# Kernel optimization log

Measured on AMD Instinct MI355X. Metric: run time of the kernel, lower is better.

The kernel has to match this reference:

```python
import jax, jax.numpy as jnp
import numpy as np

DIM = 512
HEADS = 8
HEAD_DIM = DIM // HEADS
SCALE = HEAD_DIM ** -0.5
GROUP1 = np.array([2, 3, 5, 6, 1, 4, 0, 7, 8, 9, 14, 15, 11, 12, 10, 13])
GROUP2 = np.array([0, 1, 2, 3, 5, 6, 4, 7])
EPS = 1e-5


def setup_inputs() -> dict:
    key = jax.random.key(0)
    ks = jax.random.split(key, 6)
    B, N, C = 4096, 16, DIM
    x = jax.random.normal(ks[0], (B, N, C), dtype=jnp.float32)
    w_q = jax.random.normal(ks[1], (C, C), dtype=jnp.float32) * 0.02
    w_kv = jax.random.normal(ks[2], (2 * C, C), dtype=jnp.float32) * 0.02
    w_proj = jax.random.normal(ks[3], (C, C), dtype=jnp.float32) * 0.02
    b_proj = jax.random.normal(ks[4], (C,), dtype=jnp.float32) * 0.02
    gamma = jnp.ones((C,), dtype=jnp.float32)
    beta = jnp.zeros((C,), dtype=jnp.float32)
    return {"x": x, "w_q": w_q, "w_kv": w_kv, "w_proj": w_proj,
            "b_proj": b_proj, "gamma": gamma, "beta": beta}


def _layernorm(x, gamma, beta):
    mu = jnp.mean(x, axis=-1, keepdims=True)
    var = jnp.mean(jnp.square(x - mu), axis=-1, keepdims=True)
    return (x - mu) * jax.lax.rsqrt(var + EPS) * gamma + beta


def _avg_pool_pairs(x):
    # x: (B, L, C) -> (B, L//2, C), AvgPool1d(kernel=2, stride=2) over L
    return 0.5 * (x[:, 0::2] + x[:, 1::2])


def reference(x, w_q, w_kv, w_proj, b_proj, gamma, beta):
    B, N, C = x.shape
    q = (x @ w_q.T).reshape(B, N, HEADS, HEAD_DIM).transpose(0, 2, 1, 3)  # (B,H,N,d)
    # gather + avgpool preprocessing
    p1 = _avg_pool_pairs(x[:, GROUP1])  # (B, 8, C)
    p2 = _avg_pool_pairs(x[:, GROUP2])  # (B, 4, C)
    pools = jnp.concatenate([x, p1, p2], axis=1)  # (B, N+12, C)
    pools = _layernorm(pools, gamma, beta)
    M = pools.shape[1]
    kv = (pools @ w_kv.T).reshape(B, M, 2, HEADS, HEAD_DIM).transpose(2, 0, 3, 1, 4)
    k, v = kv[0], kv[1]  # (B,H,M,d)
    attn = jax.nn.softmax(jnp.einsum('bhnd,bhmd->bhnm', q, k) * SCALE, axis=-1)
    out = jnp.einsum('bhnm,bhmd->bhnd', attn, v)  # (B,H,N,d)
    out = out.transpose(0, 2, 1, 3).reshape(B, N, C)
    return out @ w_proj.T + b_proj
```

## Files before the change

kernel.cpp:

```cpp
#include <hip/hip_runtime.h>
#include <hip/hip_bf16.h>
#include <cstdint>
#include <cstddef>


using bf16 = __hip_bfloat16;

#define B_SZ   4096
#define NTOK   16
#define CDIM   512
#define MPOOL  28
#define NHEAD  8
#define HDIM   64
#define LN_EPS 1e-5f
#define ATT_SCALE 0.125f

typedef short bf16x8 __attribute__((ext_vector_type(8)));
typedef float f32x4  __attribute__((ext_vector_type(4)));
typedef float f32x16 __attribute__((ext_vector_type(16)));

__constant__ int c_g1[16] = {2,3,5,6,1,4,0,7,8,9,14,15,11,12,10,13};
__constant__ int c_g2[8]  = {0,1,2,3,5,6,4,7};

__device__ __forceinline__ unsigned short f2b(float f) {
    unsigned u = __float_as_uint(f);
    return (unsigned short)((u + 0x7FFFu + ((u >> 16) & 1u)) >> 16);
}

__device__ __forceinline__ void lds_cp16(const void* g, void* l) {
    __builtin_amdgcn_global_load_lds(
        (const __attribute__((address_space(1))) void*)g,
        (__attribute__((address_space(3))) void*)l, 16, 0, 0);
}

__global__ __launch_bounds__(256) void convert_all_kernel(
    const float* __restrict__ w_q, const float* __restrict__ w_kv,
    const float* __restrict__ w_proj, bf16* __restrict__ wqb,
    bf16* __restrict__ wkvb, bf16* __restrict__ wpb)
{
    const float* src; bf16* dst; int i;
    const int blk = blockIdx.x;
    if (blk < 128)      { src = w_q;    dst = wqb; i = blk * 256 + threadIdx.x; }
    else if (blk < 384) { src = w_kv;   dst = wkvb; i = (blk - 128) * 256 + threadIdx.x; }
    else                { src = w_proj; dst = wpb; i = (blk - 384) * 256 + threadIdx.x; }
    const float4* p = (const float4*)(src + (size_t)i * 8);
    float4 a = p[0], b = p[1];
    uint4 pk;
    pk.x = (unsigned)f2b(a.x) | ((unsigned)f2b(a.y) << 16);
    pk.y = (unsigned)f2b(a.z) | ((unsigned)f2b(a.w) << 16);
    pk.z = (unsigned)f2b(b.x) | ((unsigned)f2b(b.y) << 16);
    pk.w = (unsigned)f2b(b.z) | ((unsigned)f2b(b.w) << 16);
    *(uint4*)(dst + (size_t)i * 8) = pk;
}

__global__ __launch_bounds__(256) void pools_ln_kernel(
    const float* __restrict__ x, const float* __restrict__ gamma,
    const float* __restrict__ beta, bf16* __restrict__ pools,
    bf16* __restrict__ xb)
{
    const int wave = threadIdx.x >> 6;
    const int lane = threadIdx.x & 63;
    const int row  = blockIdx.x * 4 + wave;
    const int b = row / MPOOL;
    const int m = row % MPOOL;
    const float* xb_src = x + (size_t)b * NTOK * CDIM;
    const int c0 = lane * 8;

    float v[8];
    if (m < 16) {
        const float4* p = (const float4*)(xb_src + m * CDIM + c0);
        float4 a = p[0], c = p[1];
        v[0]=a.x; v[1]=a.y; v[2]=a.z; v[3]=a.w;
        v[4]=c.x; v[5]=c.y; v[6]=c.z; v[7]=c.w;
        uint4 pk;
        pk.x = (unsigned)f2b(v[0]) | ((unsigned)f2b(v[1]) << 16);
        pk.y = (unsigned)f2b(v[2]) | ((unsigned)f2b(v[3]) << 16);
        pk.z = (unsigned)f2b(v[4]) | ((unsigned)f2b(v[5]) << 16);
        pk.w = (unsigned)f2b(v[6]) | ((unsigned)f2b(v[7]) << 16);
        *(uint4*)(xb + (size_t)b * NTOK * CDIM + (size_t)m * CDIM + c0) = pk;
    } else {
        int r0, r1;
        if (m < 24) { int j = m - 16; r0 = c_g1[2*j]; r1 = c_g1[2*j+1]; }
        else        { int j = m - 24; r0 = c_g2[2*j]; r1 = c_g2[2*j+1]; }
        const float4* p0 = (const float4*)(xb_src + r0 * CDIM + c0);
        const float4* p1 = (const float4*)(xb_src + r1 * CDIM + c0);
        float4 a0 = p0[0], a1 = p0[1];
        float4 b0 = p1[0], b1 = p1[1];
        v[0]=0.5f*(a0.x+b0.x); v[1]=0.5f*(a0.y+b0.y);
        v[2]=0.5f*(a0.z+b0.z); v[3]=0.5f*(a0.w+b0.w);
        v[4]=0.5f*(a1.x+b1.x); v[5]=0.5f*(a1.y+b1.y);
        v[6]=0.5f*(a1.z+b1.z); v[7]=0.5f*(a1.w+b1.w);
    }

    float s = 0.f, sq = 0.f;
#pragma unroll
    for (int j = 0; j < 8; ++j) { s += v[j]; sq += v[j]*v[j]; }
#pragma unroll
    for (int off = 1; off < 64; off <<= 1) {
        s  += __shfl_xor(s,  off, 64);
        sq += __shfl_xor(sq, off, 64);
    }
    const float mu   = s * (1.f / CDIM);
    const float var  = sq * (1.f / CDIM) - mu * mu;
    const float rstd = rsqrtf(var + LN_EPS);

    unsigned short o[8];
#pragma unroll
    for (int j = 0; j < 8; ++j) {
        float g  = gamma[c0 + j];
        float bb = beta[c0 + j];
        o[j] = f2b((v[j] - mu) * rstd * g + bb);
    }
    uint4 pk;
    pk.x = (unsigned)o[0] | ((unsigned)o[1] << 16);
    pk.y = (unsigned)o[2] | ((unsigned)o[3] << 16);
    pk.z = (unsigned)o[4] | ((unsigned)o[5] << 16);
    pk.w = (unsigned)o[6] | ((unsigned)o[7] << 16);
    *(uint4*)(pools + (size_t)row * CDIM + c0) = pk;
}

template<bool OUT_BF16, bool BIAS, int NBLK, bool FRAG32>
__global__ __launch_bounds__(512, 2) void gemm256_kernel(
    const bf16* __restrict__ A, const bf16* __restrict__ W,
    const float* __restrict__ bias, void* __restrict__ Cptr, int Ncols)
{
    constexpr int K  = 512;
    constexpr int NT = K / 32;
    extern __shared__ __align__(16) char ring[];

    const int tid = threadIdx.x;
    const int wv = tid >> 6, ln = tid & 63;
    const int wr = wv >> 2, wc = wv & 3;

    const int p  = blockIdx.x;
    const int o  = p >> 3;
    const int mb = (o / NBLK) * 8 + (p & 7);
    const int nb = o % NBLK;
    const size_t m0 = (size_t)mb * 256;
    const size_t n0 = (size_t)nb * 256;

    const int srow = wv * 16 + (ln >> 2);
    const int scol = (((ln & 3) * 16) ^ (((ln >> 3) & 3) << 4)) >> 1;
    const bf16* Asrc0 = A + (m0 + srow) * K + scol;
    const bf16* Asrc1 = A + (m0 + 128 + srow) * K + scol;
    const bf16* Wsrc0 = W + (n0 + srow) * K + scol;
    const bf16* Wsrc1 = W + (n0 + 128 + srow) * K + scol;
    char* const ringc = ring;

    auto STAGE = [&](int t) {
        char* base = ringc + (t & 3) * 32768 + wv * 1024;
        const int ko = t * 32;
        lds_cp16(Asrc0 + ko, base);
        lds_cp16(Asrc1 + ko, base + 8192);
        lds_cp16(Wsrc0 + ko, base + 16384);
        lds_cp16(Wsrc1 + ko, base + 16384 + 8192);
    };

    if constexpr (!FRAG32) {
        const int fr = ln & 15, kb = ln >> 4;
        const int aswz  = ((fr >> 1) & 3) << 4;
        const int a_off = (wr * 128 + fr) * 64 + ((kb * 16) ^ aswz);
        const int b_off = 16384 + (wc * 64 + fr) * 64 + ((kb * 16) ^ aswz);

        f32x4 acc[8][4];
#pragma unroll
        for (int i = 0; i < 8; ++i)
#pragma unroll
        for (int j = 0; j < 4; ++j)
            acc[i][j] = f32x4{0.f, 0.f, 0.f, 0.f};

        STAGE(0);
        STAGE(1);
        asm volatile("s_waitcnt vmcnt(4)" ::: "memory");
        __builtin_amdgcn_s_barrier();

#pragma unroll 1
        for (int t = 0; t < NT; ++t) {
            if (t + 2 < NT) STAGE(t + 2);
            const char* sa = ringc + (t & 3) * 32768;

            bf16x8 af[8], bfr[4];
#pragma unroll
            for (int mi = 0; mi < 8; ++mi)
                af[mi] = *(const bf16x8*)(sa + a_off + mi * 1024);
#pragma unroll
            for (int nj = 0; nj < 4; ++nj)
                bfr[nj] = *(const bf16x8*)(sa + b_off + nj * 1024);

#pragma unroll
            for (int mi = 0; mi < 8; ++mi)
#pragma unroll
            for (int nj = 0; nj < 4; ++nj)
                acc[mi][nj] = __builtin_amdgcn_mfma_f32_16x16x32_bf16(
                    af[mi], bfr[nj], acc[mi][nj], 0, 0, 0);

            if (t + 2 < NT) { asm volatile("s_waitcnt vmcnt(4)" ::: "memory"); }
            else            { asm volatile("s_waitcnt vmcnt(0)" ::: "memory"); }
            __builtin_amdgcn_s_barrier();
        }

        const int orow0 = wr * 128 + kb * 4;
        const int ocol0 = wc * 64 + fr;
        float bv[4];
#pragma unroll
        for (int nj = 0; nj < 4; ++nj)
            bv[nj] = BIAS ? bias[n0 + ocol0 + nj * 16] : 0.f;
#pragma unroll
        for (int mi = 0; mi < 8; ++mi) {
            const size_t rbase = m0 + orow0 + mi * 16;
#pragma unroll
            for (int r = 0; r < 4; ++r) {
                const size_t rowoff = (rbase + r) * (size_t)Ncols + n0 + ocol0;
#pragma unroll
                for (int nj = 0; nj < 4; ++nj) {
                    float v = acc[mi][nj][r] + bv[nj];
                    if (OUT_BF16)
                        ((unsigned short*)Cptr)[rowoff + nj * 16] = f2b(v);
                    else
                        ((float*)Cptr)[rowoff + nj * 16] = v;
                }
            }
        }
    } else {
        const int lnrow = ln & 31;
        const int khalf = ln >> 5;
        const int swz   = (((ln & 15) >> 1) & 3) << 4;
        const int a_base = (wr * 128 + lnrow) * 64;
        const int b_base = 16384 + (wc * 64 + lnrow) * 64;

        f32x16 acc[4][2];
#pragma unroll
        for (int i = 0; i < 4; ++i)
#pragma unroll
        for (int j = 0; j < 2; ++j)
#pragma unroll
            for (int e = 0; e < 16; ++e)
                acc[i][j][e] = 0.f;

        STAGE(0);
        STAGE(1);
        asm volatile("s_waitcnt vmcnt(4)" ::: "memory");
        __builtin_amdgcn_s_barrier();

#pragma unroll 1
        for (int t = 0; t < NT; ++t) {
            if (t + 2 < NT) STAGE(t + 2);
            const char* sa = ringc + (t & 3) * 32768;

            bf16x8 af[4][2], bfr[2][2];
#pragma unroll
            for (int mi = 0; mi < 4; ++mi)
#pragma unroll
                for (int ks = 0; ks < 2; ++ks)
                    af[mi][ks] = *(const bf16x8*)(sa + a_base + mi * 2048 +
                                     ((ks * 32 + khalf * 16) ^ swz));
#pragma unroll
            for (int nj = 0; nj < 2; ++nj)
#pragma unroll
                for (int ks = 0; ks < 2; ++ks)
                    bfr[nj][ks] = *(const bf16x8*)(sa + b_base + nj * 2048 +
                                     ((ks * 32 + khalf * 16) ^ swz));

#pragma unroll
            for (int mi = 0; mi < 4; ++mi)
#pragma unroll
            for (int nj = 0; nj < 2; ++nj) {
                acc[mi][nj] = __builtin_amdgcn_mfma_f32_32x32x16_bf16(
                    af[mi][0], bfr[nj][0], acc[mi][nj], 0, 0, 0);
                acc[mi][nj] = __builtin_amdgcn_mfma_f32_32x32x16_bf16(
                    af[mi][1], bfr[nj][1], acc[mi][nj], 0, 0, 0);
            }

            if (t + 2 < NT) { asm volatile("s_waitcnt vmcnt(4)" ::: "memory"); }
            else            { asm volatile("s_waitcnt vmcnt(0)" ::: "memory"); }
            __builtin_amdgcn_s_barrier();
        }

        const int ocol0 = wc * 64 + lnrow;
        float bv[2];
#pragma unroll
        for (int nj = 0; nj < 2; ++nj)
            bv[nj] = BIAS ? bias[n0 + ocol0 + nj * 32] : 0.f;
#pragma unroll
        for (int mi = 0; mi < 4; ++mi) {
            const size_t rbase = m0 + wr * 128 + mi * 32 + 4 * khalf;
#pragma unroll
            for (int r4 = 0; r4 < 4; ++r4) {
#pragma unroll
                for (int rl = 0; rl < 4; ++rl) {
                    const size_t rowoff = (rbase + rl + 8 * r4) * (size_t)Ncols
                                          + n0 + ocol0;
#pragma unroll
                    for (int nj = 0; nj < 2; ++nj) {
                        float v = acc[mi][nj][r4 * 4 + rl] + bv[nj];
                        if (OUT_BF16)
                            ((unsigned short*)Cptr)[rowoff + nj * 32] = f2b(v);
                        else
                            ((float*)Cptr)[rowoff + nj * 32] = v;
                    }
                }
            }
        }
    }
}

__global__ __launch_bounds__(256, 4) void attn_kernel(
    const bf16* __restrict__ q, const bf16* __restrict__ kv,
    bf16* __restrict__ att)
{
    extern __shared__ __align__(16) char smem[];
    char* const kvl = smem;
    unsigned short (*P_t)[512] = (unsigned short (*)[512])(smem + 32768);

    const int tid = threadIdx.x;
    const int wv = tid >> 6, ln = tid & 63;
    const int fr = ln & 15, kb = ln >> 4;
    const int b  = blockIdx.x >> 1;
    const int hg = blockIdx.x & 1;
    const int hl = wv;
    const int h  = hg * 4 + hl;

    const bf16* qb = q + (size_t)b * (NTOK * CDIM) + h * HDIM;
    bf16x8 aq[2];
#pragma unroll
    for (int ks = 0; ks < 2; ++ks)
        aq[ks] = *(const bf16x8*)(qb + fr * CDIM + ks * 32 + kb * 8);

    const char* kvg = (const char*)kv + (size_t)b * (MPOOL * 2 * CDIM * 2) + hg * 512;
    {
        const int o   = ln * 16;
        const int sb  = o >> 9;
        const int off = o & 511;
#pragma unroll
        for (int i = 0; i < 7; ++i) {
            const int row = i * 4 + wv;
            const int x   = ((row & 7) << 4) ^ (((row >> 3) & 3) << 5);
            lds_cp16(kvg + (size_t)row * 2048 + sb * 1024 + (off ^ x),
                     kvl + row * 1024);
        }
    }
    *(uint4*)(kvl + 28672 + tid * 16) = uint4{0u, 0u, 0u, 0u};
    __syncthreads();

    bf16x8 bk[2][2];
#pragma unroll
    for (int mt = 0; mt < 2; ++mt) {
        const int row = mt * 16 + fr;
        const int x   = ((row & 7) << 4) ^ (((row >> 3) & 3) << 5);
#pragma unroll
        for (int ks = 0; ks < 2; ++ks)
            bk[mt][ks] = *(const bf16x8*)(kvl + row * 1024 +
                              ((hl * 128 + ks * 64 + kb * 16) ^ x));
    }

    bf16x8 bv[4];
#pragma unroll
    for (int dt = 0; dt < 4; ++dt)
#pragma unroll
        for (int j = 0; j < 8; ++j) {
            const int row = kb * 8 + j;
            const int x   = ((row & 7) << 4) ^ (((row >> 3) & 3) << 5);
            bv[dt][j] = *(const short*)(kvl + row * 1024 + 512 +
                              ((hl * 128 + dt * 32 + fr * 2) ^ x));
        }

    f32x4 st0 = {0.f, 0.f, 0.f, 0.f}, st1 = {0.f, 0.f, 0.f, 0.f};
    st0 = __builtin_amdgcn_mfma_f32_16x16x32_bf16(aq[0], bk[0][0], st0, 0, 0, 0);
    st0 = __builtin_amdgcn_mfma_f32_16x16x32_bf16(aq[1], bk[0][1], st0, 0, 0, 0);
    st1 = __builtin_amdgcn_mfma_f32_16x16x32_bf16(aq[0], bk[1][0], st1, 0, 0, 0);
    st1 = __builtin_amdgcn_mfma_f32_16x16x32_bf16(aq[1], bk[1][1], st1, 0, 0, 0);

    const bool kmask = (fr >= MPOOL - 16);
#pragma unroll
    for (int r = 0; r < 4; ++r) {
        st0[r] *= ATT_SCALE;
        st1[r] = kmask ? -1e30f : st1[r] * ATT_SCALE;
    }

    float p0[4], p1[4];
#pragma unroll
    for (int r = 0; r < 4; ++r) {
        float mx = fmaxf(st0[r], st1[r]);
        mx = fmaxf(mx, __shfl_xor(mx, 1, 64));
        mx = fmaxf(mx, __shfl_xor(mx, 2, 64));
        mx = fmaxf(mx, __shfl_xor(mx, 4, 64));
        mx = fmaxf(mx, __shfl_xor(mx, 8, 64));
        float e0 = expf(st0[r] - mx);
        float e1 = expf(st1[r] - mx);
        float s = e0 + e1;
        s += __shfl_xor(s, 1, 64);
        s += __shfl_xor(s, 2, 64);
        s += __shfl_xor(s, 4, 64);
        s += __shfl_xor(s, 8, 64);
        const float inv = 1.f / s;
        p0[r] = e0 * inv;
        p1[r] = e1 * inv;
    }

    {
        ushort4 w0, w1;
        w0.x = f2b(p0[0]); w0.y = f2b(p0[1]); w0.z = f2b(p0[2]); w0.w = f2b(p0[3]);
        w1.x = f2b(p1[0]); w1.y = f2b(p1[1]); w1.z = f2b(p1[2]); w1.w = f2b(p1[3]);
        *(ushort4*)&P_t[wv][(fr)      * 16 + kb * 4] = w0;
        *(ushort4*)&P_t[wv][(16 + fr) * 16 + kb * 4] = w1;
    }
    asm volatile("s_waitcnt lgkmcnt(0)" ::: "memory");

    bf16x8 pa;
#pragma unroll
    for (int j = 0; j < 8; ++j)
        pa[j] = (short)P_t[wv][(kb * 8 + j) * 16 + fr];

    f32x4 o[4];
#pragma unroll
    for (int dt = 0; dt < 4; ++dt) {
        o[dt] = f32x4{0.f, 0.f, 0.f, 0.f};
        o[dt] = __builtin_amdgcn_mfma_f32_16x16x32_bf16(pa, bv[dt], o[dt], 0, 0, 0);
    }

    unsigned short* ob = (unsigned short*)(att + (size_t)b * (NTOK * CDIM) + h * HDIM);
#pragma unroll
    for (int r = 0; r < 4; ++r) {
        const size_t nrow = (size_t)(kb * 4 + r) * CDIM;
#pragma unroll
        for (int dt = 0; dt < 4; ++dt)
            ob[nrow + dt * 16 + fr] = f2b(o[dt][r]);
    }
}

extern "C" void kernel_launch(void* const* d_in, const int* in_sizes, int n_in,
                              void* d_out, int out_size, void* d_ws, size_t ws_size,
                              hipStream_t stream)
{
    const float* x      = (const float*)d_in[0];
    const float* w_q    = (const float*)d_in[1];
    const float* w_kv   = (const float*)d_in[2];
    const float* w_proj = (const float*)d_in[3];
    const float* b_proj = (const float*)d_in[4];
    const float* gamma  = (const float*)d_in[5];
    const float* beta   = (const float*)d_in[6];

    char* ws = (char*)d_ws;
    bf16* xb    = (bf16*)(ws);
    bf16* pools = (bf16*)(ws + 67108864ull);
    bf16* qbuf  = (bf16*)(ws + 67108864ull + 117440512ull);
    bf16* kvbuf = (bf16*)(ws + 67108864ull + 117440512ull + 67108864ull);
    bf16* wqb   = (bf16*)(ws + 67108864ull + 117440512ull + 67108864ull + 234881024ull);
    bf16* wkvb  = (bf16*)((char*)wqb + 524288ull);
    bf16* wpb   = (bf16*)((char*)wkvb + 1048576ull);
    bf16* atbuf = pools;

    hipFuncSetAttribute((const void*)gemm256_kernel<true, false, 2, false>,
                        hipFuncAttributeMaxDynamicSharedMemorySize, 131072);
    hipFuncSetAttribute((const void*)gemm256_kernel<true, false, 4, true>,
                        hipFuncAttributeMaxDynamicSharedMemorySize, 131072);
    hipFuncSetAttribute((const void*)gemm256_kernel<false, true, 2, false>,
                        hipFuncAttributeMaxDynamicSharedMemorySize, 131072);
    hipFuncSetAttribute((const void*)attn_kernel,
                        hipFuncAttributeMaxDynamicSharedMemorySize, 36864);

    convert_all_kernel<<<512, 256, 0, stream>>>(w_q, w_kv, w_proj, wqb, wkvb, wpb);

    pools_ln_kernel<<<(B_SZ * MPOOL) / 4, 256, 0, stream>>>(x, gamma, beta, pools, xb);

    gemm256_kernel<true, false, 2, false><<<512, 512, 131072, stream>>>(
        xb, wqb, nullptr, (void*)qbuf, 512);

    gemm256_kernel<true, false, 4, true><<<1792, 512, 131072, stream>>>(
        pools, wkvb, nullptr, (void*)kvbuf, 1024);

    attn_kernel<<<B_SZ * 2, 256, 36864, stream>>>(qbuf, kvbuf, atbuf);

    gemm256_kernel<false, true, 2, false><<<512, 512, 131072, stream>>>(
        atbuf, wpb, b_proj, d_out, 512);
}
```

Measured before the change: 420.1 us.

## Switch GEMM pipeline to double-buffered 64-wide K tiles with fewer barriers

```diff
diff --git a/kernel.cpp b/kernel.cpp
--- a/kernel.cpp
+++ b/kernel.cpp
@@ -125,7 +125,7 @@
     const float* __restrict__ bias, void* __restrict__ Cptr, int Ncols)
 {
     constexpr int K  = 512;
-    constexpr int NT = K / 32;
+    constexpr int NT = K / 64;
     extern __shared__ __align__(16) char ring[];
 
     const int tid = threadIdx.x;
@@ -148,19 +148,24 @@
     char* const ringc = ring;
 
     auto STAGE = [&](int t) {
-        char* base = ringc + (t & 3) * 32768 + wv * 1024;
-        const int ko = t * 32;
-        lds_cp16(Asrc0 + ko, base);
-        lds_cp16(Asrc1 + ko, base + 8192);
-        lds_cp16(Wsrc0 + ko, base + 16384);
-        lds_cp16(Wsrc1 + ko, base + 16384 + 8192);
+        char* base = ringc + (t & 1) * 65536 + wv * 1024;
+        const int ko = t * 64;
+#pragma unroll
+        for (int ksub = 0; ksub < 2; ++ksub) {
+            char* sb = base + ksub * 16384;
+            const int kc = ko + ksub * 32;
+            lds_cp16(Asrc0 + kc, sb);
+            lds_cp16(Asrc1 + kc, sb + 8192);
+            lds_cp16(Wsrc0 + kc, sb + 32768);
+            lds_cp16(Wsrc1 + kc, sb + 32768 + 8192);
+        }
     };
 
     if constexpr (!FRAG32) {
         const int fr = ln & 15, kb = ln >> 4;
-        const int aswz  = ((fr >> 1) & 3) << 4;
-        const int a_off = (wr * 128 + fr) * 64 + ((kb * 16) ^ aswz);
-        const int b_off = 16384 + (wc * 64 + fr) * 64 + ((kb * 16) ^ aswz);
+        const int aswz = ((fr >> 1) & 3) << 4;
+        const int a_in = (wr * 128 + fr) * 64 + ((kb * 16) ^ aswz);
+        const int b_in = (wc * 64 + fr) * 64 + ((kb * 16) ^ aswz);
 
         f32x4 acc[8][4];
 #pragma unroll
@@ -170,33 +175,39 @@
             acc[i][j] = f32x4{0.f, 0.f, 0.f, 0.f};
 
         STAGE(0);
-        STAGE(1);
-        asm volatile("s_waitcnt vmcnt(4)" ::: "memory");
+        asm volatile("s_waitcnt vmcnt(0)" ::: "memory");
         __builtin_amdgcn_s_barrier();
 
 #pragma unroll 1
         for (int t = 0; t < NT; ++t) {
-            if (t + 2 < NT) STAGE(t + 2);
-            const char* sa = ringc + (t & 3) * 32768;
-
-            bf16x8 af[8], bfr[4];
-#pragma unroll
-            for (int mi = 0; mi < 8; ++mi)
-                af[mi] = *(const bf16x8*)(sa + a_off + mi * 1024);
-#pragma unroll
-            for (int nj = 0; nj < 4; ++nj)
-                bfr[nj] = *(const bf16x8*)(sa + b_off + nj * 1024);
-
-#pragma unroll
-            for (int mi = 0; mi < 8; ++mi)
-#pragma unroll
-            for (int nj = 0; nj < 4; ++nj)
-                acc[mi][nj] = __builtin_amdgcn_mfma_f32_16x16x32_bf16(
-                    af[mi], bfr[nj], acc[mi][nj], 0, 0, 0);
-
-            if (t + 2 < NT) { asm volatile("s_waitcnt vmcnt(4)" ::: "memory"); }
-            else            { asm volatile("s_waitcnt vmcnt(0)" ::: "memory"); }
-            __builtin_amdgcn_s_barrier();
+            if (t + 1 < NT) STAGE(t + 1);
+            const char* sa = ringc + (t & 1) * 65536;
+
+#pragma unroll
+            for (int ksub = 0; ksub < 2; ++ksub) {
+                const char* ssA = sa + ksub * 16384;
+                const char* ssB = sa + 32768 + ksub * 16384;
+
+                bf16x8 af[8], bfr[4];
+#pragma unroll
+                for (int mi = 0; mi < 8; ++mi)
+                    af[mi] = *(const bf16x8*)(ssA + a_in + mi * 1024);
+#pragma unroll
+                for (int nj = 0; nj < 4; ++nj)
+                    bfr[nj] = *(const bf16x8*)(ssB + b_in + nj * 1024);
+
+#pragma unroll
+                for (int mi = 0; mi < 8; ++mi)
+#pragma unroll
+                for (int nj = 0; nj < 4; ++nj)
+                    acc[mi][nj] = __builtin_amdgcn_mfma_f32_16x16x32_bf16(
+                        af[mi], bfr[nj], acc[mi][nj], 0, 0, 0);
+            }
+
+            if (t + 1 < NT) {
+                asm volatile("s_waitcnt vmcnt(0)" ::: "memory");
+                __builtin_amdgcn_s_barrier();
+            }
         }
 
         const int orow0 = wr * 128 + kb * 4;
@@ -225,8 +236,8 @@
         const int lnrow = ln & 31;
         const int khalf = ln >> 5;
         const int swz   = (((ln & 15) >> 1) & 3) << 4;
-        const int a_base = (wr * 128 + lnrow) * 64;
-        const int b_base = 16384 + (wc * 64 + lnrow) * 64;
+        const int a_in = (wr * 128 + lnrow) * 64;
+        const int b_in = (wc * 64 + lnrow) * 64;
 
         f32x16 acc[4][2];
 #pragma unroll
@@ -238,42 +249,48 @@
                 acc[i][j][e] = 0.f;
 
         STAGE(0);
-        STAGE(1);
-        asm volatile("s_waitcnt vmcnt(4)" ::: "memory");
+        asm volatile("s_waitcnt vmcnt(0)" ::: "memory");
         __builtin_amdgcn_s_barrier();
 
 #pragma unroll 1
         for (int t = 0; t < NT; ++t) {
-            if (t + 2 < NT) STAGE(t + 2);
-            const char* sa = ringc + (t & 3) * 32768;
-
-            bf16x8 af[4][2], bfr[2][2];
-#pragma unroll
-            for (int mi = 0; mi < 4; ++mi)
-#pragma unroll
-                for (int ks = 0; ks < 2; ++ks)
-                    af[mi][ks] = *(const bf16x8*)(sa + a_base + mi * 2048 +
-                                     ((ks * 32 + khalf * 16) ^ swz));
-#pragma unroll
-            for (int nj = 0; nj < 2; ++nj)
-#pragma unroll
-                for (int ks = 0; ks < 2; ++ks)
-                    bfr[nj][ks] = *(const bf16x8*)(sa + b_base + nj * 2048 +
-                                     ((ks * 32 + khalf * 16) ^ swz));
-
-#pragma unroll
-            for (int mi = 0; mi < 4; ++mi)
-#pragma unroll
-            for (int nj = 0; nj < 2; ++nj) {
-                acc[mi][nj] = __builtin_amdgcn_mfma_f32_32x32x16_bf16(
-                    af[mi][0], bfr[nj][0], acc[mi][nj], 0, 0, 0);
-                acc[mi][nj] = __builtin_amdgcn_mfma_f32_32x32x16_bf16(
-                    af[mi][1], bfr[nj][1], acc[mi][nj], 0, 0, 0);
-            }
-
-            if (t + 2 < NT) { asm volatile("s_waitcnt vmcnt(4)" ::: "memory"); }
-            else            { asm volatile("s_waitcnt vmcnt(0)" ::: "memory"); }
-            __builtin_amdgcn_s_barrier();
+            if (t + 1 < NT) STAGE(t + 1);
+            const char* sa = ringc + (t & 1) * 65536;
+
+#pragma unroll
+            for (int ksub = 0; ksub < 2; ++ksub) {
+                const char* ssA = sa + ksub * 16384;
+                const char* ssB = sa + 32768 + ksub * 16384;
+
+                bf16x8 af[4][2], bfr[2][2];
+#pragma unroll
+                for (int mi = 0; mi < 4; ++mi)
+#pragma unroll
+                    for (int ks = 0; ks < 2; ++ks)
+                        af[mi][ks] = *(const bf16x8*)(ssA + a_in + mi * 2048 +
+                                         ((ks * 32 + khalf * 16) ^ swz));
+#pragma unroll
+                for (int nj = 0; nj < 2; ++nj)
+#pragma unroll
+                    for (int ks = 0; ks < 2; ++ks)
+                        bfr[nj][ks] = *(const bf16x8*)(ssB + b_in + nj * 2048 +
+                                         ((ks * 32 + khalf * 16) ^ swz));
+
+#pragma unroll
+                for (int mi = 0; mi < 4; ++mi)
+#pragma unroll
+                for (int nj = 0; nj < 2; ++nj) {
+                    acc[mi][nj] = __builtin_amdgcn_mfma_f32_32x32x16_bf16(
+                        af[mi][0], bfr[nj][0], acc[mi][nj], 0, 0, 0);
+                    acc[mi][nj] = __builtin_amdgcn_mfma_f32_32x32x16_bf16(
+                        af[mi][1], bfr[nj][1], acc[mi][nj], 0, 0, 0);
+                }
+            }
+
+            if (t + 1 < NT) {
+                asm volatile("s_waitcnt vmcnt(0)" ::: "memory");
+                __builtin_amdgcn_s_barrier();
+            }
         }
 
         const int ocol0 = wc * 64 + lnrow;
```

Result: slower. 434.4 us (+3.4%).
